# Optimization experiments

Measured on AMD Instinct MI355X. Metric: run time of the kernel, lower is better.

The kernel has to match this reference:

```python
import jax, jax.numpy as jnp
import numpy as np

B, SEQ, EMB, HID = 256, 256, 128, 512
NG = 1          # n_glimpses
CEXP = 10.0     # tanh_exploration
NEG = -1e9      # masked-logit value (stands in for -inf)


def setup_inputs():
    key = jax.random.key(0)
    ks = jax.random.split(key, 19)
    se = 1.0 / np.sqrt(EMB)
    sh = 1.0 / np.sqrt(HID)
    u = lambda k, shape, s: jax.random.uniform(k, shape, jnp.float32, -s, s)
    return {
        'embedding': u(ks[0], (SEQ, EMB), 1.0),
        'enc_Wih': u(ks[1], (4 * HID, EMB), sh),
        'enc_Whh': u(ks[2], (4 * HID, HID), sh),
        'enc_b': u(ks[3], (4 * HID,), sh),
        'dec_Wih': u(ks[4], (4 * HID, EMB), sh),
        'dec_Whh': u(ks[5], (4 * HID, HID), sh),
        'dec_b': u(ks[6], (4 * HID,), sh),
        'pt_Wq': u(ks[7], (HID, HID), sh), 'pt_bq': u(ks[8], (HID,), sh),
        'pt_Wref': u(ks[9], (HID, HID), sh), 'pt_bref': u(ks[10], (HID,), sh),
        'pt_V': u(ks[11], (HID,), sh),
        'gl_Wq': u(ks[12], (HID, HID), sh), 'gl_bq': u(ks[13], (HID,), sh),
        'gl_Wref': u(ks[14], (HID, HID), sh), 'gl_bref': u(ks[15], (HID,), sh),
        'gl_V': u(ks[16], (HID,), sh),
        'dec_start': u(ks[17], (EMB,), se),
        'inputs': jax.random.randint(ks[18], (B, SEQ), 0, SEQ),
    }


def lstm_cell(x, h, c, Wih, Whh, b):
    # PyTorch gate order: i, f, g, o
    g = x @ Wih.T + h @ Whh.T + b
    i, f, gg, o = jnp.split(g, 4, axis=1)
    c = jax.nn.sigmoid(f) * c + jax.nn.sigmoid(i) * jnp.tanh(gg)
    h = jax.nn.sigmoid(o) * jnp.tanh(c)
    return h, c


def reference(embedding, enc_Wih, enc_Whh, enc_b,
              dec_Wih, dec_Whh, dec_b,
              pt_Wq, pt_bq, pt_Wref, pt_bref, pt_V,
              gl_Wq, gl_bq, gl_Wref, gl_bref, gl_V,
              dec_start, inputs):
    emb = embedding[inputs]                      # [B,S,E]
    h0 = jnp.zeros((B, HID), jnp.float32)
    c0 = jnp.zeros((B, HID), jnp.float32)

    def enc_step(carry, x_t):
        h, c = carry
        h, c = lstm_cell(x_t, h, c, enc_Wih, enc_Whh, enc_b)
        return (h, c), h

    (h, c), hs = jax.lax.scan(enc_step, (h0, c0), jnp.swapaxes(emb, 0, 1))
    enc_out = jnp.swapaxes(hs, 0, 1)             # [B,S,H]

    # W_ref is a 1x1 Conv1d == per-position linear; precompute once (constant across steps)
    gl_ref = enc_out @ gl_Wref.T + gl_bref       # [B,S,H]
    pt_ref = enc_out @ pt_Wref.T + pt_bref       # [B,S,H]

    keys = jax.random.split(jax.random.key(1), SEQ)
    mask0 = jnp.zeros((B, SEQ), bool)
    dec_in0 = jnp.broadcast_to(dec_start, (B, EMB))

    def dec_step(carry, key_i):
        h, c, mask, dec_in = carry
        h, c = lstm_cell(dec_in, h, c, dec_Wih, dec_Whh, dec_b)
        q = h                                    # [B,H]
        for _ in range(NG):
            gl = jnp.tanh((q @ gl_Wq.T + gl_bq)[:, None, :] + gl_ref) @ gl_V  # [B,S]
            gl = jnp.where(mask, NEG, gl)
            q = jnp.einsum('bsh,bs->bh', gl_ref, jax.nn.softmax(gl, axis=1))
        lg = jnp.tanh((q @ pt_Wq.T + pt_bq)[:, None, :] + pt_ref) @ pt_V      # [B,S]
        lg = CEXP * jnp.tanh(lg)                 # use_tanh=True pointer
        lg = jnp.where(mask, NEG, lg)
        # Categorical sample via Gumbel-max
        gum = -jnp.log(-jnp.log(jax.random.uniform(key_i, (B, SEQ)) + 1e-10) + 1e-10)
        ptr = jnp.argmax(lg + gum, axis=1)       # [B]
        logp = jnp.take_along_axis(jax.nn.log_softmax(lg, axis=1), ptr[:, None], axis=1)[:, 0]
        mask = mask.at[jnp.arange(B), ptr].set(True)
        dec_in = emb[jnp.arange(B), ptr]         # embedding of chosen city
        return (h, c, mask, dec_in), (ptr, logp)

    _, (tours, logps) = jax.lax.scan(dec_step, (h, c, mask0, dec_in0), keys)
    return jnp.swapaxes(tours, 0, 1), jnp.swapaxes(logps, 0, 1)  # [B,S] each
```

## Files before the change

### kernel.cpp

```cpp
#include <hip/hip_runtime.h>
#include <math.h>


#define Bz 256
#define Sz 256
#define Ez 128
#define Hz 512
#define NEGV -1e9f
#define BH (Bz*Hz)

__device__ float g_encout[Bz*Sz*Hz];
__device__ float g_glref[Bz*Sz*Hz];
__device__ float g_ptref[Bz*Sz*Hz];
__device__ float g_xpe[256*2048];
__device__ float g_xpd[257*2048];
__device__ float g_h[2*BH];
__device__ float g_c[BH];
__device__ int g_ptrbuf[Bz];
__device__ unsigned g_keys[2*Sz];
__device__ unsigned char g_mask[Bz*Sz];

__device__ __forceinline__ unsigned rotl32(unsigned v, int d){ return (v<<d)|(v>>(32-d)); }

__device__ __forceinline__ void tf2x32(unsigned k0, unsigned k1, unsigned x0, unsigned x1,
                                       unsigned &o0, unsigned &o1){
  unsigned ks2 = k0 ^ k1 ^ 0x1BD11BDAu;
  x0 += k0; x1 += k1;
#define TFR(r) { x0 += x1; x1 = rotl32(x1,(r)); x1 ^= x0; }
  TFR(13) TFR(15) TFR(26) TFR(6)
  x0 += k1; x1 += ks2 + 1u;
  TFR(17) TFR(29) TFR(16) TFR(24)
  x0 += ks2; x1 += k0 + 2u;
  TFR(13) TFR(15) TFR(26) TFR(6)
  x0 += k0; x1 += k1 + 3u;
  TFR(17) TFR(29) TFR(16) TFR(24)
  x0 += k1; x1 += ks2 + 4u;
  TFR(13) TFR(15) TFR(26) TFR(6)
  x0 += ks2; x1 += k0 + 5u;
#undef TFR
  o0 = x0; o1 = x1;
}

__device__ __forceinline__ unsigned rng_bits(unsigned ka, unsigned kb, unsigned idx){
  unsigned o0,o1; tf2x32(ka,kb, 0u, idx, o0,o1);
  return o0 ^ o1;
}

__global__ __launch_bounds__(256) void init_kernel(){
  int i = blockIdx.x*256 + threadIdx.x;
  if (i < BH){ g_h[i] = 0.f; g_c[i] = 0.f; }
  if (i < Bz*Sz) g_mask[i] = 0;
  if (i < Sz){
    unsigned o0,o1; tf2x32(0u,1u, 0u, (unsigned)i, o0,o1);
    g_keys[2*i] = o0; g_keys[2*i+1] = o1;
  }
}

__global__ __launch_bounds__(256) void xproj_kernel(
    const float* __restrict__ Wih, const float* __restrict__ bias,
    const float* __restrict__ emb, const float* __restrict__ dstart,
    int dst)
{
  float* Xp = dst ? g_xpd : g_xpe;
  int c = blockIdx.x;
  int row = blockIdx.y*256 + threadIdx.x;
  __shared__ float xs[Ez];
  if (threadIdx.x < Ez) xs[threadIdx.x] = (c < 256) ? emb[c*Ez + threadIdx.x]
                                                    : dstart[threadIdx.x];
  __syncthreads();
  float a = bias[row];
  const float* w = Wih + (size_t)row*Ez;
  #pragma unroll 8
  for (int k = 0; k < Ez; k++) a = fmaf(xs[k], w[k], a);
  Xp[(size_t)c*2048 + row] = a;
}

__global__ __launch_bounds__(256) void lstm_step(
    const float* __restrict__ Whh,
    const int*   __restrict__ inputs,
    int t, int is_dec, int hsel)
{
  __shared__ float A_lds[32][36];
  __shared__ float W_lds[64][36];

  const float* h_in = g_h + (size_t)hsel*BH;
  float*       h_out = g_h + (size_t)(hsel^1)*BH;
  const float* Xp = is_dec ? g_xpd : g_xpe;

  int tid = threadIdx.x;
  int bt = blockIdx.x;
  int jt = blockIdx.y;
  int jj = tid & 15;
  int bp = tid >> 4;
  int jglob = jt*16 + jj;

  int bA = bt*32 + bp*2, bB = bA + 1;
  int cA, cB;
  if (is_dec){
    if (t == 0){ cA = 256; cB = 256; }
    else { cA = inputs[bA*Sz + g_ptrbuf[bA]]; cB = inputs[bB*Sz + g_ptrbuf[bB]]; }
  } else {
    cA = inputs[bA*Sz + t]; cB = inputs[bB*Sz + t];
  }

  float acc[2][4];
  {
    const float* xa = Xp + (size_t)cA*2048;
    const float* xb = Xp + (size_t)cB*2048;
    #pragma unroll
    for (int g=0; g<4; g++){
      acc[0][g] = xa[g*Hz + jglob];
      acc[1][g] = xb[g*Hz + jglob];
    }
  }

  int sr = tid >> 3;
  int sk = (tid & 7) * 4;
  int wr = tid >> 2;
  int wk = (tid & 3) * 8;
  int bg = bt*32 + sr;
  int wrow_g = (wr >> 4)*Hz + jt*16 + (wr & 15);

  for (int kc = 0; kc < 16; kc++){
    int k0 = kc*32;
    __syncthreads();
    {
      float4 av = *(const float4*)(h_in + (size_t)bg*Hz + k0 + sk);
      *(float4*)&A_lds[sr][sk] = av;
    }
    {
      const float* ws = Whh + (size_t)wrow_g*Hz + k0 + wk;
      float4 w0 = *(const float4*)ws;
      float4 w1 = *(const float4*)(ws + 4);
      *(float4*)&W_lds[wr][wk]     = w0;
      *(float4*)&W_lds[wr][wk + 4] = w1;
    }
    __syncthreads();
    #pragma unroll
    for (int k4 = 0; k4 < 8; k4++){
      float4 w0 = *(const float4*)&W_lds[jj      ][k4*4];
      float4 w1 = *(const float4*)&W_lds[16 + jj ][k4*4];
      float4 w2 = *(const float4*)&W_lds[32 + jj ][k4*4];
      float4 w3 = *(const float4*)&W_lds[48 + jj ][k4*4];
      float4 a0 = *(const float4*)&A_lds[bp*2    ][k4*4];
      float4 a1 = *(const float4*)&A_lds[bp*2 + 1][k4*4];
#define LSTEP(c) \
      acc[0][0]=fmaf(a0.c,w0.c,acc[0][0]); acc[0][1]=fmaf(a0.c,w1.c,acc[0][1]); \
      acc[0][2]=fmaf(a0.c,w2.c,acc[0][2]); acc[0][3]=fmaf(a0.c,w3.c,acc[0][3]); \
      acc[1][0]=fmaf(a1.c,w0.c,acc[1][0]); acc[1][1]=fmaf(a1.c,w1.c,acc[1][1]); \
      acc[1][2]=fmaf(a1.c,w2.c,acc[1][2]); acc[1][3]=fmaf(a1.c,w3.c,acc[1][3]);
      LSTEP(x) LSTEP(y) LSTEP(z) LSTEP(w)
#undef LSTEP
    }
  }

  #pragma unroll
  for (int r=0;r<2;r++){
    int b = bA + r;
    float gi = acc[r][0], gf = acc[r][1], gg = acc[r][2], go = acc[r][3];
    float co = g_c[(size_t)b*Hz + jglob];
    float si = 1.f/(1.f + expf(-gi));
    float sf = 1.f/(1.f + expf(-gf));
    float so = 1.f/(1.f + expf(-go));
    float cn = sf*co + si*tanhf(gg);
    float hn = so*tanhf(cn);
    g_c[(size_t)b*Hz + jglob] = cn;
    h_out[(size_t)b*Hz + jglob] = hn;
    if (!is_dec) g_encout[((size_t)b*Sz + t)*Hz + jglob] = hn;
  }
}

__global__ __launch_bounds__(256) void gemm_ref(
    const float* __restrict__ W, const float* __restrict__ bias, int dst_id)
{
  const float* A = g_encout;
  float*       C = (dst_id == 1) ? g_glref : g_ptref;
  __shared__ float As[32][68];
  __shared__ float Ws[32][68];
  int tid = threadIdx.x;
  int mt = blockIdx.x * 64, nt = blockIdx.y * 64;
  int tm = (tid & 15) * 4, tn = (tid >> 4) * 4;
  float acc[4][4] = {};
  int lr = tid >> 2;
  int lk = (tid & 3) * 8;

  for (int kc = 0; kc < 16; kc++){
    int k0 = kc*32;
    __syncthreads();
    {
      const float* ar = A + (size_t)(mt + lr)*Hz + k0 + lk;
      float4 a0 = *(const float4*)ar, a1 = *(const float4*)(ar+4);
      As[lk+0][lr]=a0.x; As[lk+1][lr]=a0.y; As[lk+2][lr]=a0.z; As[lk+3][lr]=a0.w;
      As[lk+4][lr]=a1.x; As[lk+5][lr]=a1.y; As[lk+6][lr]=a1.z; As[lk+7][lr]=a1.w;
      const float* wrp = W + (size_t)(nt + lr)*Hz + k0 + lk;
      float4 w0 = *(const float4*)wrp, w1 = *(const float4*)(wrp+4);
      Ws[lk+0][lr]=w0.x; Ws[lk+1][lr]=w0.y; Ws[lk+2][lr]=w0.z; Ws[lk+3][lr]=w0.w;
      Ws[lk+4][lr]=w1.x; Ws[lk+5][lr]=w1.y; Ws[lk+6][lr]=w1.z; Ws[lk+7][lr]=w1.w;
    }
    __syncthreads();
    #pragma unroll
    for (int k=0;k<32;k++){
      float4 av = *(const float4*)&As[k][tm];
      float4 wv = *(const float4*)&Ws[k][tn];
      acc[0][0]=fmaf(av.x,wv.x,acc[0][0]); acc[0][1]=fmaf(av.x,wv.y,acc[0][1]);
      acc[0][2]=fmaf(av.x,wv.z,acc[0][2]); acc[0][3]=fmaf(av.x,wv.w,acc[0][3]);
      acc[1][0]=fmaf(av.y,wv.x,acc[1][0]); acc[1][1]=fmaf(av.y,wv.y,acc[1][1]);
      acc[1][2]=fmaf(av.y,wv.z,acc[1][2]); acc[1][3]=fmaf(av.y,wv.w,acc[1][3]);
      acc[2][0]=fmaf(av.z,wv.x,acc[2][0]); acc[2][1]=fmaf(av.z,wv.y,acc[2][1]);
      acc[2][2]=fmaf(av.z,wv.z,acc[2][2]); acc[2][3]=fmaf(av.z,wv.w,acc[2][3]);
      acc[3][0]=fmaf(av.w,wv.x,acc[3][0]); acc[3][1]=fmaf(av.w,wv.y,acc[3][1]);
      acc[3][2]=fmaf(av.w,wv.z,acc[3][2]); acc[3][3]=fmaf(av.w,wv.w,acc[3][3]);
    }
  }
  float b0v = bias[nt+tn+0], b1v = bias[nt+tn+1], b2v = bias[nt+tn+2], b3v = bias[nt+tn+3];
  #pragma unroll
  for (int i=0;i<4;i++){
    float4 o;
    o.x = acc[i][0] + b0v; o.y = acc[i][1] + b1v;
    o.z = acc[i][2] + b2v; o.w = acc[i][3] + b3v;
    *(float4*)(C + (size_t)(mt + tm + i)*Hz + nt + tn) = o;
  }
}

__global__ __launch_bounds__(512) void attn_step(
    const float* __restrict__ gl_Wq, const float* __restrict__ gl_bq,
    const float* __restrict__ gl_V,
    const float* __restrict__ pt_Wq, const float* __restrict__ pt_bq,
    const float* __restrict__ pt_V,
    int t, int hsel2, float* __restrict__ out)
{
  int b = blockIdx.x, tid = threadIdx.x;
  int wave = tid >> 6, lane64 = tid & 63;
  int g = tid >> 5, lane = tid & 31;

  __shared__ __align__(16) float hq[Hz];
  __shared__ __align__(16) float q2s[Hz];
  __shared__ __align__(16) float qgs[Hz];
  __shared__ __align__(16) float qps[Hz];
  __shared__ __align__(16) float vgl[Hz];
  __shared__ __align__(16) float vpt[Hz];
  __shared__ float part[16][513];
  __shared__ float m_arr[16];
  __shared__ float l_arr[16];
  __shared__ int   rlist[16][16];
  __shared__ float slog[Sz];
  __shared__ float redy[8]; __shared__ int redi[8];
  __shared__ float redm[8]; __shared__ float redsum[8];

  hq[tid]  = g_h[(size_t)hsel2*BH + (size_t)b*Hz + tid];
  vgl[tid] = gl_V[tid];
  vpt[tid] = pt_V[tid];
  __syncthreads();

  const unsigned char* mrow = g_mask + b*Sz;

  int cnt;
  {
    bool un = (lane < 16) ? (mrow[g*16 + lane] == 0) : false;
    unsigned long long bal = __ballot(un);
    unsigned m16 = (unsigned)((g & 1) ? (bal >> 32) : bal) & 0xFFFFu;
    cnt = __popc(m16);
    if (lane < 16){
      if (un){
        int rank = __popc(m16 & ((1u << lane) - 1u));
        rlist[g][rank] = g*16 + lane;
      } else {
        slog[g*16 + lane] = NEGV;
      }
    }
  }

  {
    float hv[8];
    #pragma unroll
    for (int i=0;i<8;i++) hv[i] = hq[lane64*8 + i];
    for (int jj=0;jj<64;jj+=2){
      int j0 = wave*64 + jj;
      const float* wr0 = gl_Wq + (size_t)j0*Hz + lane64*8;
      const float* wr1 = wr0 + Hz;
      float4 A0 = *(const float4*)wr0, A1 = *(const float4*)(wr0+4);
      float4 B0 = *(const float4*)wr1, B1 = *(const float4*)(wr1+4);
      float p0 = 0.f, p1 = 0.f;
      p0 = fmaf(hv[0], A0.x, p0); p0 = fmaf(hv[1], A0.y, p0);
      p0 = fmaf(hv[2], A0.z, p0); p0 = fmaf(hv[3], A0.w, p0);
      p0 = fmaf(hv[4], A1.x, p0); p0 = fmaf(hv[5], A1.y, p0);
      p0 = fmaf(hv[6], A1.z, p0); p0 = fmaf(hv[7], A1.w, p0);
      p1 = fmaf(hv[0], B0.x, p1); p1 = fmaf(hv[1], B0.y, p1);
      p1 = fmaf(hv[2], B0.z, p1); p1 = fmaf(hv[3], B0.w, p1);
      p1 = fmaf(hv[4], B1.x, p1); p1 = fmaf(hv[5], B1.y, p1);
      p1 = fmaf(hv[6], B1.z, p1); p1 = fmaf(hv[7], B1.w, p1);
      #pragma unroll
      for (int off=32; off; off>>=1) p0 += __shfl_xor(p0, off);
      #pragma unroll
      for (int off=32; off; off>>=1) p1 += __shfl_xor(p1, off);
      if (lane64 == 0){ q2s[j0] = p0 + gl_bq[j0]; q2s[j0+1] = p1 + gl_bq[j0+1]; }
    }
  }
  __syncthreads();

  const float* glbase = g_glref + (size_t)b*Sz*Hz;
  {
    float m_g = -INFINITY, l_g = 0.f;
    float4 racc[4];
    { float4 z = {0.f,0.f,0.f,0.f}; racc[0]=z; racc[1]=z; racc[2]=z; racc[3]=z; }

    float4 xn0, xn1, xn2, xn3;
    if (cnt > 0){
      const float4* rp = (const float4*)(glbase + (size_t)rlist[g][0]*Hz);
      xn0 = rp[lane]; xn1 = rp[lane+32]; xn2 = rp[lane+64]; xn3 = rp[lane+96];
    }
    for (int i = 0; i < cnt; i++){
      float4 x0 = xn0, x1 = xn1, x2 = xn2, x3 = xn3;
      if (i + 1 < cnt){
        const float4* rp = (const float4*)(glbase + (size_t)rlist[g][i+1]*Hz);
        xn0 = rp[lane]; xn1 = rp[lane+32]; xn2 = rp[lane+64]; xn3 = rp[lane+96];
      }
      float p = 0.f;
      {
        float4 q, vv;
        q = *(const float4*)&q2s[lane*4];        vv = *(const float4*)&vgl[lane*4];
        p = fmaf(vv.x, tanhf(q.x + x0.x), p); p = fmaf(vv.y, tanhf(q.y + x0.y), p);
        p = fmaf(vv.z, tanhf(q.z + x0.z), p); p = fmaf(vv.w, tanhf(q.w + x0.w), p);
        q = *(const float4*)&q2s[(lane+32)*4];   vv = *(const float4*)&vgl[(lane+32)*4];
        p = fmaf(vv.x, tanhf(q.x + x1.x), p); p = fmaf(vv.y, tanhf(q.y + x1.y), p);
        p = fmaf(vv.z, tanhf(q.z + x1.z), p); p = fmaf(vv.w, tanhf(q.w + x1.w), p);
        q = *(const float4*)&q2s[(lane+64)*4];   vv = *(const float4*)&vgl[(lane+64)*4];
        p = fmaf(vv.x, tanhf(q.x + x2.x), p); p = fmaf(vv.y, tanhf(q.y + x2.y), p);
        p = fmaf(vv.z, tanhf(q.z + x2.z), p); p = fmaf(vv.w, tanhf(q.w + x2.w), p);
        q = *(const float4*)&q2s[(lane+96)*4];   vv = *(const float4*)&vgl[(lane+96)*4];
        p = fmaf(vv.x, tanhf(q.x + x3.x), p); p = fmaf(vv.y, tanhf(q.y + x3.y), p);
        p = fmaf(vv.z, tanhf(q.z + x3.z), p); p = fmaf(vv.w, tanhf(q.w + x3.w), p);
      }
      #pragma unroll
      for (int off=16; off; off>>=1) p += __shfl_xor(p, off, 32);
      float lgv = p;
      if (lgv > m_g){
        float r_ = expf(m_g - lgv);
        l_g *= r_;
        racc[0].x*=r_; racc[0].y*=r_; racc[0].z*=r_; racc[0].w*=r_;
        racc[1].x*=r_; racc[1].y*=r_; racc[1].z*=r_; racc[1].w*=r_;
        racc[2].x*=r_; racc[2].y*=r_; racc[2].z*=r_; racc[2].w*=r_;
        racc[3].x*=r_; racc[3].y*=r_; racc[3].z*=r_; racc[3].w*=r_;
        m_g = lgv;
      }
      float pr = expf(lgv - m_g);
      l_g += pr;
      racc[0].x=fmaf(pr,x0.x,racc[0].x); racc[0].y=fmaf(pr,x0.y,racc[0].y);
      racc[0].z=fmaf(pr,x0.z,racc[0].z); racc[0].w=fmaf(pr,x0.w,racc[0].w);
      racc[1].x=fmaf(pr,x1.x,racc[1].x); racc[1].y=fmaf(pr,x1.y,racc[1].y);
      racc[1].z=fmaf(pr,x1.z,racc[1].z); racc[1].w=fmaf(pr,x1.w,racc[1].w);
      racc[2].x=fmaf(pr,x2.x,racc[2].x); racc[2].y=fmaf(pr,x2.y,racc[2].y);
      racc[2].z=fmaf(pr,x2.z,racc[2].z); racc[2].w=fmaf(pr,x2.w,racc[2].w);
      racc[3].x=fmaf(pr,x3.x,racc[3].x); racc[3].y=fmaf(pr,x3.y,racc[3].y);
      racc[3].z=fmaf(pr,x3.z,racc[3].z); racc[3].w=fmaf(pr,x3.w,racc[3].w);
    }
    if (lane == 0){ m_arr[g] = m_g; l_arr[g] = l_g; }
    part[g][4*lane+  0] = racc[0].x; part[g][4*lane+  1] = racc[0].y;
    part[g][4*lane+  2] = racc[0].z; part[g][4*lane+  3] = racc[0].w;
    part[g][4*lane+128] = racc[1].x; part[g][4*lane+129] = racc[1].y;
    part[g][4*lane+130] = racc[1].z; part[g][4*lane+131] = racc[1].w;
    part[g][4*lane+256] = racc[2].x; part[g][4*lane+257] = racc[2].y;
    part[g][4*lane+258] = racc[2].z; part[g][4*lane+259] = racc[2].w;
    part[g][4*lane+384] = racc[3].x; part[g][4*lane+385] = racc[3].y;
    part[g][4*lane+386] = racc[3].z; part[g][4*lane+387] = racc[3].w;
  }
  __syncthreads();

  {
    float M = m_arr[0];
    #pragma unroll
    for (int gg=1; gg<16; gg++) M = fmaxf(M, m_arr[gg]);
    float num = 0.f, den = 0.f;
    #pragma unroll
    for (int gg=0; gg<16; gg++){
      float w = expf(m_arr[gg] - M);
      num = fmaf(w, part[gg][tid], num);
      den = fmaf(w, l_arr[gg], den);
    }
    qgs[tid] = num / den;
  }
  __syncthreads();

  {
    float qv[8];
    #pragma unroll
    for (int i=0;i<8;i++) qv[i] = qgs[lane64*8 + i];
    for (int jj=0;jj<64;jj+=2){
      int j0 = wave*64 + jj;
      const float* wr0 = pt_Wq + (size_t)j0*Hz + lane64*8;
      const float* wr1 = wr0 + Hz;
      float4 A0 = *(const float4*)wr0, A1 = *(const float4*)(wr0+4);
      float4 B0 = *(const float4*)wr1, B1 = *(const float4*)(wr1+4);
      float p0 = 0.f, p1 = 0.f;
      p0 = fmaf(qv[0], A0.x, p0); p0 = fmaf(qv[1], A0.y, p0);
      p0 = fmaf(qv[2], A0.z, p0); p0 = fmaf(qv[3], A0.w, p0);
      p0 = fmaf(qv[4], A1.x, p0); p0 = fmaf(qv[5], A1.y, p0);
      p0 = fmaf(qv[6], A1.z, p0); p0 = fmaf(qv[7], A1.w, p0);
      p1 = fmaf(qv[0], B0.x, p1); p1 = fmaf(qv[1], B0.y, p1);
      p1 = fmaf(qv[2], B0.z, p1); p1 = fmaf(qv[3], B0.w, p1);
      p1 = fmaf(qv[4], B1.x, p1); p1 = fmaf(qv[5], B1.y, p1);
      p1 = fmaf(qv[6], B1.z, p1); p1 = fmaf(qv[7], B1.w, p1);
      #pragma unroll
      for (int off=32; off; off>>=1) p0 += __shfl_xor(p0, off);
      #pragma unroll
      for (int off=32; off; off>>=1) p1 += __shfl_xor(p1, off);
      if (lane64 == 0){ qps[j0] = p0 + pt_bq[j0]; qps[j0+1] = p1 + pt_bq[j0+1]; }
    }
  }
  __syncthreads();

  const float* ptbase = g_ptref + (size_t)b*Sz*Hz;
  {
    float4 xn0, xn1, xn2, xn3;
    if (cnt > 0){
      const float4* rp = (const float4*)(ptbase + (size_t)rlist[g][0]*Hz);
      xn0 = rp[lane]; xn1 = rp[lane+32]; xn2 = rp[lane+64]; xn3 = rp[lane+96];
    }
    for (int i = 0; i < cnt; i++){
      int s = rlist[g][i];
      float4 x0 = xn0, x1 = xn1, x2 = xn2, x3 = xn3;
      if (i + 1 < cnt){
        const float4* rp = (const float4*)(ptbase + (size_t)rlist[g][i+1]*Hz);
        xn0 = rp[lane]; xn1 = rp[lane+32]; xn2 = rp[lane+64]; xn3 = rp[lane+96];
      }
      float p = 0.f;
      {
        float4 q, vv;
        q = *(const float4*)&qps[lane*4];        vv = *(const float4*)&vpt[lane*4];
        p = fmaf(vv.x, tanhf(q.x + x0.x), p); p = fmaf(vv.y, tanhf(q.y + x0.y), p);
        p = fmaf(vv.z, tanhf(q.z + x0.z), p); p = fmaf(vv.w, tanhf(q.w + x0.w), p);
        q = *(const float4*)&qps[(lane+32)*4];   vv = *(const float4*)&vpt[(lane+32)*4];
        p = fmaf(vv.x, tanhf(q.x + x1.x), p); p = fmaf(vv.y, tanhf(q.y + x1.y), p);
        p = fmaf(vv.z, tanhf(q.z + x1.z), p); p = fmaf(vv.w, tanhf(q.w + x1.w), p);
        q = *(const float4*)&qps[(lane+64)*4];   vv = *(const float4*)&vpt[(lane+64)*4];
        p = fmaf(vv.x, tanhf(q.x + x2.x), p); p = fmaf(vv.y, tanhf(q.y + x2.y), p);
        p = fmaf(vv.z, tanhf(q.z + x2.z), p); p = fmaf(vv.w, tanhf(q.w + x2.w), p);
        q = *(const float4*)&qps[(lane+96)*4];   vv = *(const float4*)&vpt[(lane+96)*4];
        p = fmaf(vv.x, tanhf(q.x + x3.x), p); p = fmaf(vv.y, tanhf(q.y + x3.y), p);
        p = fmaf(vv.z, tanhf(q.z + x3.z), p); p = fmaf(vv.w, tanhf(q.w + x3.w), p);
      }
      #pragma unroll
      for (int off=16; off; off>>=1) p += __shfl_xor(p, off, 32);
      if (lane == 0) slog[s] = 10.f * tanhf(p);
    }
  }
  __syncthreads();

  float lg = NEGV, y = -INFINITY;
  if (tid < Sz){
    lg = slog[tid];
    unsigned bits = rng_bits(g_keys[2*t], g_keys[2*t+1], (unsigned)(b*Sz + tid));
    float u = __uint_as_float((bits >> 9) | 0x3f800000u) - 1.f;
    float gum = -logf(-logf(u + 1e-10f) + 1e-10f);
    y = lg + gum;
  }
  float by = y; int bi = tid; float bm = lg;
  #pragma unroll
  for (int off=32; off; off>>=1){
    float oy = __shfl_xor(by, off);
    int   oi = __shfl_xor(bi, off);
    float om = __shfl_xor(bm, off);
    if (oy > by || (oy == by && oi < bi)){ by = oy; bi = oi; }
    bm = fmaxf(bm, om);
  }
  if (lane64 == 0){ redy[wave] = by; redi[wave] = bi; redm[wave] = bm; }
  __syncthreads();
  float fy = redy[0]; int fi = redi[0]; float fm = redm[0];
  #pragma unroll
  for (int w=1; w<8; w++){
    if (redy[w] > fy || (redy[w] == fy && redi[w] < fi)){ fy = redy[w]; fi = redi[w]; }
    fm = fmaxf(fm, redm[w]);
  }
  int ptr = fi;

  float pe = (tid < Sz) ? expf(lg - fm) : 0.f;
  #pragma unroll
  for (int off=32; off; off>>=1) pe += __shfl_xor(pe, off);
  if (lane64 == 0) redsum[wave] = pe;
  __syncthreads();
  if (tid == 0){
    float den = ((redsum[0]+redsum[1]) + (redsum[2]+redsum[3]))
              + ((redsum[4]+redsum[5]) + (redsum[6]+redsum[7]));
    float logp = slog[ptr] - fm - logf(den);
    out[(size_t)b*Sz + t] = (float)ptr;
    out[(size_t)Bz*Sz + (size_t)b*Sz + t] = logp;
    g_mask[b*Sz + ptr] = 1;
    g_ptrbuf[b] = ptr;
  }
}

extern "C" void kernel_launch(void* const* d_in, const int* in_sizes, int n_in,
                              void* d_out, int out_size, void* d_ws, size_t ws_size,
                              hipStream_t stream){
  (void)in_sizes; (void)n_in; (void)out_size; (void)d_ws; (void)ws_size;
  const float* embedding = (const float*)d_in[0];
  const float* enc_Wih = (const float*)d_in[1];
  const float* enc_Whh = (const float*)d_in[2];
  const float* enc_b   = (const float*)d_in[3];
  const float* dec_Wih = (const float*)d_in[4];
  const float* dec_Whh = (const float*)d_in[5];
  const float* dec_b   = (const float*)d_in[6];
  const float* pt_Wq   = (const float*)d_in[7];
  const float* pt_bq   = (const float*)d_in[8];
  const float* pt_Wref = (const float*)d_in[9];
  const float* pt_bref = (const float*)d_in[10];
  const float* pt_V    = (const float*)d_in[11];
  const float* gl_Wq   = (const float*)d_in[12];
  const float* gl_bq   = (const float*)d_in[13];
  const float* gl_Wref = (const float*)d_in[14];
  const float* gl_bref = (const float*)d_in[15];
  const float* gl_V    = (const float*)d_in[16];
  const float* dec_start = (const float*)d_in[17];
  const int*   inputs  = (const int*)d_in[18];
  float* out = (float*)d_out;

  init_kernel<<<512, 256, 0, stream>>>();
  xproj_kernel<<<dim3(256,8), 256, 0, stream>>>(enc_Wih, enc_b, embedding, dec_start, 0);
  xproj_kernel<<<dim3(257,8), 256, 0, stream>>>(dec_Wih, dec_b, embedding, dec_start, 1);

  for (int t = 0; t < Sz; t++){
    lstm_step<<<dim3(8,32), 256, 0, stream>>>(enc_Whh, inputs, t, 0, t & 1);
  }
  gemm_ref<<<dim3(1024,8), 256, 0, stream>>>(gl_Wref, gl_bref, 1);
  gemm_ref<<<dim3(1024,8), 256, 0, stream>>>(pt_Wref, pt_bref, 2);

  for (int t = 0; t < Sz; t++){
    lstm_step<<<dim3(8,32), 256, 0, stream>>>(dec_Whh, inputs, t, 1, t & 1);
    attn_step<<<Bz, 512, 0, stream>>>(gl_Wq, gl_bq, gl_V,
        pt_Wq, pt_bq, pt_V, t, (t+1) & 1, out);
  }
}
```

Baseline: 34.79 ms.

## Double threads per block in LSTM step and attention step kernels

Changes the LSTM step kernel to 512 threads so each thread computes one batch row of four gates instead of two. The attention kernel goes to 1024 threads with 32 groups of 8 sequence positions each, halving per-thread work in the query projections and logit loops. Query and V vectors are hoisted into registers out of the inner logit loop. The aim is more parallelism and latency hiding in the small per-step kernels, at the cost of higher register pressure, larger shared-memory partial buffers, and a 32-way merge.

```diff
diff --git a/kernel.cpp b/kernel.cpp
--- a/kernel.cpp
+++ b/kernel.cpp
@@ -75,7 +75,7 @@
   Xp[(size_t)c*2048 + row] = a;
 }
 
-__global__ __launch_bounds__(256) void lstm_step(
+__global__ __launch_bounds__(512) void lstm_step(
     const float* __restrict__ Whh,
     const int*   __restrict__ inputs,
     int t, int is_dec, int hsel)
@@ -93,47 +93,34 @@
   int jj = tid & 15;
   int bp = tid >> 4;
   int jglob = jt*16 + jj;
-
-  int bA = bt*32 + bp*2, bB = bA + 1;
-  int cA, cB;
-  if (is_dec){
-    if (t == 0){ cA = 256; cB = 256; }
-    else { cA = inputs[bA*Sz + g_ptrbuf[bA]]; cB = inputs[bB*Sz + g_ptrbuf[bB]]; }
-  } else {
-    cA = inputs[bA*Sz + t]; cB = inputs[bB*Sz + t];
-  }
-
-  float acc[2][4];
+  int b = bt*32 + bp;
+
+  int c;
+  if (is_dec) c = (t == 0) ? 256 : inputs[b*Sz + g_ptrbuf[b]];
+  else        c = inputs[b*Sz + t];
+
+  float acc[4];
   {
-    const float* xa = Xp + (size_t)cA*2048;
-    const float* xb = Xp + (size_t)cB*2048;
-    #pragma unroll
-    for (int g=0; g<4; g++){
-      acc[0][g] = xa[g*Hz + jglob];
-      acc[1][g] = xb[g*Hz + jglob];
-    }
+    const float* xa = Xp + (size_t)c*2048;
+    #pragma unroll
+    for (int g=0; g<4; g++) acc[g] = xa[g*Hz + jglob];
   }
 
   int sr = tid >> 3;
   int sk = (tid & 7) * 4;
-  int wr = tid >> 2;
-  int wk = (tid & 3) * 8;
-  int bg = bt*32 + sr;
-  int wrow_g = (wr >> 4)*Hz + jt*16 + (wr & 15);
+  int wrow_g = (sr >> 4)*Hz + jt*16 + (sr & 15);
 
   for (int kc = 0; kc < 16; kc++){
     int k0 = kc*32;
     __syncthreads();
+    if (tid < 256){
+      float4 av = *(const float4*)(h_in + (size_t)(bt*32 + (tid>>3))*Hz + k0 + sk);
+      *(float4*)&A_lds[tid>>3][sk] = av;
+    }
     {
-      float4 av = *(const float4*)(h_in + (size_t)bg*Hz + k0 + sk);
-      *(float4*)&A_lds[sr][sk] = av;
-    }
-    {
-      const float* ws = Whh + (size_t)wrow_g*Hz + k0 + wk;
+      const float* ws = Whh + (size_t)wrow_g*Hz + k0 + sk;
       float4 w0 = *(const float4*)ws;
-      float4 w1 = *(const float4*)(ws + 4);
-      *(float4*)&W_lds[wr][wk]     = w0;
-      *(float4*)&W_lds[wr][wk + 4] = w1;
+      *(float4*)&W_lds[sr][sk] = w0;
     }
     __syncthreads();
     #pragma unroll
@@ -142,32 +129,25 @@
       float4 w1 = *(const float4*)&W_lds[16 + jj ][k4*4];
       float4 w2 = *(const float4*)&W_lds[32 + jj ][k4*4];
       float4 w3 = *(const float4*)&W_lds[48 + jj ][k4*4];
-      float4 a0 = *(const float4*)&A_lds[bp*2    ][k4*4];
-      float4 a1 = *(const float4*)&A_lds[bp*2 + 1][k4*4];
-#define LSTEP(c) \
-      acc[0][0]=fmaf(a0.c,w0.c,acc[0][0]); acc[0][1]=fmaf(a0.c,w1.c,acc[0][1]); \
-      acc[0][2]=fmaf(a0.c,w2.c,acc[0][2]); acc[0][3]=fmaf(a0.c,w3.c,acc[0][3]); \
-      acc[1][0]=fmaf(a1.c,w0.c,acc[1][0]); acc[1][1]=fmaf(a1.c,w1.c,acc[1][1]); \
-      acc[1][2]=fmaf(a1.c,w2.c,acc[1][2]); acc[1][3]=fmaf(a1.c,w3.c,acc[1][3]);
+      float4 a0 = *(const float4*)&A_lds[bp][k4*4];
+#define LSTEP(c_) \
+      acc[0]=fmaf(a0.c_,w0.c_,acc[0]); acc[1]=fmaf(a0.c_,w1.c_,acc[1]); \
+      acc[2]=fmaf(a0.c_,w2.c_,acc[2]); acc[3]=fmaf(a0.c_,w3.c_,acc[3]);
       LSTEP(x) LSTEP(y) LSTEP(z) LSTEP(w)
 #undef LSTEP
     }
   }
 
-  #pragma unroll
-  for (int r=0;r<2;r++){
-    int b = bA + r;
-    float gi = acc[r][0], gf = acc[r][1], gg = acc[r][2], go = acc[r][3];
-    float co = g_c[(size_t)b*Hz + jglob];
-    float si = 1.f/(1.f + expf(-gi));
-    float sf = 1.f/(1.f + expf(-gf));
-    float so = 1.f/(1.f + expf(-go));
-    float cn = sf*co + si*tanhf(gg);
-    float hn = so*tanhf(cn);
-    g_c[(size_t)b*Hz + jglob] = cn;
-    h_out[(size_t)b*Hz + jglob] = hn;
-    if (!is_dec) g_encout[((size_t)b*Sz + t)*Hz + jglob] = hn;
-  }
+  float gi = acc[0], gf = acc[1], gg = acc[2], go = acc[3];
+  float co = g_c[(size_t)b*Hz + jglob];
+  float si = 1.f/(1.f + expf(-gi));
+  float sf = 1.f/(1.f + expf(-gf));
+  float so = 1.f/(1.f + expf(-go));
+  float cn = sf*co + si*tanhf(gg);
+  float hn = so*tanhf(cn);
+  g_c[(size_t)b*Hz + jglob] = cn;
+  h_out[(size_t)b*Hz + jglob] = hn;
+  if (!is_dec) g_encout[((size_t)b*Sz + t)*Hz + jglob] = hn;
 }
 
 __global__ __launch_bounds__(256) void gemm_ref(
@@ -222,7 +202,24 @@
   }
 }
 
-__global__ __launch_bounds__(512) void attn_step(
+__device__ __forceinline__ float logit_chain(
+    const float4& x0, const float4& x1, const float4& x2, const float4& x3,
+    const float4& q0, const float4& q1, const float4& q2, const float4& q3,
+    const float4& v0, const float4& v1, const float4& v2, const float4& v3)
+{
+  float p = 0.f;
+  p = fmaf(v0.x, tanhf(q0.x + x0.x), p); p = fmaf(v0.y, tanhf(q0.y + x0.y), p);
+  p = fmaf(v0.z, tanhf(q0.z + x0.z), p); p = fmaf(v0.w, tanhf(q0.w + x0.w), p);
+  p = fmaf(v1.x, tanhf(q1.x + x1.x), p); p = fmaf(v1.y, tanhf(q1.y + x1.y), p);
+  p = fmaf(v1.z, tanhf(q1.z + x1.z), p); p = fmaf(v1.w, tanhf(q1.w + x1.w), p);
+  p = fmaf(v2.x, tanhf(q2.x + x2.x), p); p = fmaf(v2.y, tanhf(q2.y + x2.y), p);
+  p = fmaf(v2.z, tanhf(q2.z + x2.z), p); p = fmaf(v2.w, tanhf(q2.w + x2.w), p);
+  p = fmaf(v3.x, tanhf(q3.x + x3.x), p); p = fmaf(v3.y, tanhf(q3.y + x3.y), p);
+  p = fmaf(v3.z, tanhf(q3.z + x3.z), p); p = fmaf(v3.w, tanhf(q3.w + x3.w), p);
+  return p;
+}
+
+__global__ __launch_bounds__(1024) void attn_step(
     const float* __restrict__ gl_Wq, const float* __restrict__ gl_bq,
     const float* __restrict__ gl_V,
     const float* __restrict__ pt_Wq, const float* __restrict__ pt_bq,
@@ -239,33 +236,35 @@
   __shared__ __align__(16) float qps[Hz];
   __shared__ __align__(16) float vgl[Hz];
   __shared__ __align__(16) float vpt[Hz];
-  __shared__ float part[16][513];
-  __shared__ float m_arr[16];
-  __shared__ float l_arr[16];
-  __shared__ int   rlist[16][16];
+  __shared__ float part[32][513];
+  __shared__ float m_arr[32];
+  __shared__ float l_arr[32];
+  __shared__ int   rlist[32][8];
   __shared__ float slog[Sz];
-  __shared__ float redy[8]; __shared__ int redi[8];
-  __shared__ float redm[8]; __shared__ float redsum[8];
-
-  hq[tid]  = g_h[(size_t)hsel2*BH + (size_t)b*Hz + tid];
-  vgl[tid] = gl_V[tid];
-  vpt[tid] = pt_V[tid];
+  __shared__ float redy[16]; __shared__ int redi[16];
+  __shared__ float redm[16]; __shared__ float redsum[16];
+
+  if (tid < Hz){
+    hq[tid]  = g_h[(size_t)hsel2*BH + (size_t)b*Hz + tid];
+    vgl[tid] = gl_V[tid];
+    vpt[tid] = pt_V[tid];
+  }
   __syncthreads();
 
   const unsigned char* mrow = g_mask + b*Sz;
 
   int cnt;
   {
-    bool un = (lane < 16) ? (mrow[g*16 + lane] == 0) : false;
+    bool un = (lane < 8) ? (mrow[g*8 + lane] == 0) : false;
     unsigned long long bal = __ballot(un);
-    unsigned m16 = (unsigned)((g & 1) ? (bal >> 32) : bal) & 0xFFFFu;
-    cnt = __popc(m16);
-    if (lane < 16){
+    unsigned m8 = (unsigned)(bal >> ((g & 1) ? 32 : 0)) & 0xFFu;
+    cnt = __popc(m8);
+    if (lane < 8){
       if (un){
-        int rank = __popc(m16 & ((1u << lane) - 1u));
-        rlist[g][rank] = g*16 + lane;
+        int rank = __popc(m8 & ((1u << lane) - 1u));
+        rlist[g][rank] = g*8 + lane;
       } else {
-        slog[g*16 + lane] = NEGV;
+        slog[g*8 + lane] = NEGV;
       }
     }
   }
@@ -274,8 +273,8 @@
     float hv[8];
     #pragma unroll
     for (int i=0;i<8;i++) hv[i] = hq[lane64*8 + i];
-    for (int jj=0;jj<64;jj+=2){
-      int j0 = wave*64 + jj;
+    for (int jj=0;jj<32;jj+=2){
+      int j0 = wave*32 + jj;
       const float* wr0 = gl_Wq + (size_t)j0*Hz + lane64*8;
       const float* wr1 = wr0 + Hz;
       float4 A0 = *(const float4*)wr0, A1 = *(const float4*)(wr0+4);
@@ -300,6 +299,15 @@
 
   const float* glbase = g_glref + (size_t)b*Sz*Hz;
   {
+    float4 q0 = *(const float4*)&q2s[lane*4];
+    float4 q1 = *(const float4*)&q2s[(lane+32)*4];
+    float4 q2 = *(const float4*)&q2s[(lane+64)*4];
+    float4 q3 = *(const float4*)&q2s[(lane+96)*4];
+    float4 v0 = *(const float4*)&vgl[lane*4];
+    float4 v1 = *(const float4*)&vgl[(lane+32)*4];
+    float4 v2 = *(const float4*)&vgl[(lane+64)*4];
+    float4 v3 = *(const float4*)&vgl[(lane+96)*4];
+
     float m_g = -INFINITY, l_g = 0.f;
     float4 racc[4];
     { float4 z = {0.f,0.f,0.f,0.f}; racc[0]=z; racc[1]=z; racc[2]=z; racc[3]=z; }
@@ -315,22 +323,7 @@
         const float4* rp = (const float4*)(glbase + (size_t)rlist[g][i+1]*Hz);
         xn0 = rp[lane]; xn1 = rp[lane+32]; xn2 = rp[lane+64]; xn3 = rp[lane+96];
       }
-      float p = 0.f;
-      {
-        float4 q, vv;
-        q = *(const float4*)&q2s[lane*4];        vv = *(const float4*)&vgl[lane*4];
-        p = fmaf(vv.x, tanhf(q.x + x0.x), p); p = fmaf(vv.y, tanhf(q.y + x0.y), p);
-        p = fmaf(vv.z, tanhf(q.z + x0.z), p); p = fmaf(vv.w, tanhf(q.w + x0.w), p);
-        q = *(const float4*)&q2s[(lane+32)*4];   vv = *(const float4*)&vgl[(lane+32)*4];
-        p = fmaf(vv.x, tanhf(q.x + x1.x), p); p = fmaf(vv.y, tanhf(q.y + x1.y), p);
-        p = fmaf(vv.z, tanhf(q.z + x1.z), p); p = fmaf(vv.w, tanhf(q.w + x1.w), p);
-        q = *(const float4*)&q2s[(lane+64)*4];   vv = *(const float4*)&vgl[(lane+64)*4];
-        p = fmaf(vv.x, tanhf(q.x + x2.x), p); p = fmaf(vv.y, tanhf(q.y + x2.y), p);
-        p = fmaf(vv.z, tanhf(q.z + x2.z), p); p = fmaf(vv.w, tanhf(q.w + x2.w), p);
-        q = *(const float4*)&q2s[(lane+96)*4];   vv = *(const float4*)&vgl[(lane+96)*4];
-        p = fmaf(vv.x, tanhf(q.x + x3.x), p); p = fmaf(vv.y, tanhf(q.y + x3.y), p);
-        p = fmaf(vv.z, tanhf(q.z + x3.z), p); p = fmaf(vv.w, tanhf(q.w + x3.w), p);
-      }
+      float p = logit_chain(x0,x1,x2,x3, q0,q1,q2,q3, v0,v1,v2,v3);
       #pragma unroll
       for (int off=16; off; off>>=1) p += __shfl_xor(p, off, 32);
       float lgv = p;
@@ -366,13 +359,13 @@
   }
   __syncthreads();
 
-  {
+  if (tid < Hz){
     float M = m_arr[0];
     #pragma unroll
-    for (int gg=1; gg<16; gg++) M = fmaxf(M, m_arr[gg]);
+    for (int gg=1; gg<32; gg++) M = fmaxf(M, m_arr[gg]);
     float num = 0.f, den = 0.f;
     #pragma unroll
-    for (int gg=0; gg<16; gg++){
+    for (int gg=0; gg<32; gg++){
       float w = expf(m_arr[gg] - M);
       num = fmaf(w, part[gg][tid], num);
       den = fmaf(w, l_arr[gg], den);
@@ -385,8 +378,8 @@
     float qv[8];
     #pragma unroll
     for (int i=0;i<8;i++) qv[i] = qgs[lane64*8 + i];
-    for (int jj=0;jj<64;jj+=2){
-      int j0 = wave*64 + jj;
+    for (int jj=0;jj<32;jj+=2){
+      int j0 = wave*32 + jj;
       const float* wr0 = pt_Wq + (size_t)j0*Hz + lane64*8;
       const float* wr1 = wr0 + Hz;
       float4 A0 = *(const float4*)wr0, A1 = *(const float4*)(wr0+4);
@@ -411,6 +404,15 @@
 
   const float* ptbase = g_ptref + (size_t)b*Sz*Hz;
   {
+    float4 q0 = *(const float4*)&qps[lane*4];
+    float4 q1 = *(const float4*)&qps[(lane+32)*4];
+    float4 q2 = *(const float4*)&qps[(lane+64)*4];
+    float4 q3 = *(const float4*)&qps[(lane+96)*4];
+    float4 v0 = *(const float4*)&vpt[lane*4];
+    float4 v1 = *(const float4*)&vpt[(lane+32)*4];
+    float4 v2 = *(const float4*)&vpt[(lane+64)*4];
+    float4 v3 = *(const float4*)&vpt[(lane+96)*4];
+
     float4 xn0, xn1, xn2, xn3;
     if (cnt > 0){
       const float4* rp = (const float4*)(ptbase + (size_t)rlist[g][0]*Hz);
@@ -423,22 +425,7 @@
         const float4* rp = (const float4*)(ptbase + (size_t)rlist[g][i+1]*Hz);
         xn0 = rp[lane]; xn1 = rp[lane+32]; xn2 = rp[lane+64]; xn3 = rp[lane+96];
       }
-      float p = 0.f;
-      {
-        float4 q, vv;
-        q = *(const float4*)&qps[lane*4];        vv = *(const float4*)&vpt[lane*4];
-        p = fmaf(vv.x, tanhf(q.x + x0.x), p); p = fmaf(vv.y, tanhf(q.y + x0.y), p);
-        p = fmaf(vv.z, tanhf(q.z + x0.z), p); p = fmaf(vv.w, tanhf(q.w + x0.w), p);
-        q = *(const float4*)&qps[(lane+32)*4];   vv = *(const float4*)&vpt[(lane+32)*4];
-        p = fmaf(vv.x, tanhf(q.x + x1.x), p); p = fmaf(vv.y, tanhf(q.y + x1.y), p);
-        p = fmaf(vv.z, tanhf(q.z + x1.z), p); p = fmaf(vv.w, tanhf(q.w + x1.w), p);
-        q = *(const float4*)&qps[(lane+64)*4];   vv = *(const float4*)&vpt[(lane+64)*4];
-        p = fmaf(vv.x, tanhf(q.x + x2.x), p); p = fmaf(vv.y, tanhf(q.y + x2.y), p);
-        p = fmaf(vv.z, tanhf(q.z + x2.z), p); p = fmaf(vv.w, tanhf(q.w + x2.w), p);
-        q = *(const float4*)&qps[(lane+96)*4];   vv = *(const float4*)&vpt[(lane+96)*4];
-        p = fmaf(vv.x, tanhf(q.x + x3.x), p); p = fmaf(vv.y, tanhf(q.y + x3.y), p);
-        p = fmaf(vv.z, tanhf(q.z + x3.z), p); p = fmaf(vv.w, tanhf(q.w + x3.w), p);
-      }
+      float p = logit_chain(x0,x1,x2,x3, q0,q1,q2,q3, v0,v1,v2,v3);
       #pragma unroll
       for (int off=16; off; off>>=1) p += __shfl_xor(p, off, 32);
       if (lane == 0) slog[s] = 10.f * tanhf(p);
@@ -467,7 +454,7 @@
   __syncthreads();
   float fy = redy[0]; int fi = redi[0]; float fm = redm[0];
   #pragma unroll
-  for (int w=1; w<8; w++){
+  for (int w=1; w<16; w++){
     if (redy[w] > fy || (redy[w] == fy && redi[w] < fi)){ fy = redy[w]; fi = redi[w]; }
     fm = fmaxf(fm, redm[w]);
   }
@@ -479,8 +466,9 @@
   if (lane64 == 0) redsum[wave] = pe;
   __syncthreads();
   if (tid == 0){
-    float den = ((redsum[0]+redsum[1]) + (redsum[2]+redsum[3]))
-              + ((redsum[4]+redsum[5]) + (redsum[6]+redsum[7]));
+    float den = 0.f;
+    #pragma unroll
+    for (int w=0; w<16; w++) den += redsum[w];
     float logp = slog[ptr] - fm - logf(den);
     out[(size_t)b*Sz + t] = (float)ptr;
     out[(size_t)Bz*Sz + (size_t)b*Sz + t] = logp;
@@ -519,14 +507,14 @@
   xproj_kernel<<<dim3(257,8), 256, 0, stream>>>(dec_Wih, dec_b, embedding, dec_start, 1);
 
   for (int t = 0; t < Sz; t++){
-    lstm_step<<<dim3(8,32), 256, 0, stream>>>(enc_Whh, inputs, t, 0, t & 1);
+    lstm_step<<<dim3(8,32), 512, 0, stream>>>(enc_Whh, inputs, t, 0, t & 1);
   }
   gemm_ref<<<dim3(1024,8), 256, 0, stream>>>(gl_Wref, gl_bref, 1);
   gemm_ref<<<dim3(1024,8), 256, 0, stream>>>(pt_Wref, pt_bref, 2);
 
   for (int t = 0; t < Sz; t++){
-    lstm_step<<<dim3(8,32), 256, 0, stream>>>(dec_Whh, inputs, t, 1, t & 1);
-    attn_step<<<Bz, 512, 0, stream>>>(gl_Wq, gl_bq, gl_V,
+    lstm_step<<<dim3(8,32), 512, 0, stream>>>(dec_Whh, inputs, t, 1, t & 1);
+    attn_step<<<Bz, 1024, 0, stream>>>(gl_Wq, gl_bq, gl_V,
         pt_Wq, pt_bq, pt_V, t, (t+1) & 1, out);
   }
 }
```

After: 37.67 ms. 1.08x slower.
